# Kernel tuning notes

Measured on AMD Instinct MI355X. Metric: run time of the kernel, lower is better.

Reference implementation:

```python
import jax, jax.numpy as jnp
import numpy as np

NUM_NODES = 64
NUM_FEATURES = 256
OUTPUT_DIM = 256
BATCH_GRAPHS = 4096
TOTAL_ROWS = NUM_NODES * BATCH_GRAPHS


def setup_inputs() -> dict:
    key = jax.random.key(0)
    kx, kw = jax.random.split(key)
    x = jax.random.normal(kx, (TOTAL_ROWS, NUM_FEATURES), dtype=jnp.float32)
    # row i belongs to graph i // NUM_NODES (matches stride-num_nodes indexing in the module)
    batch = jnp.arange(TOTAL_ROWS, dtype=jnp.int64) // NUM_NODES
    # per-node linear weights: mlp[inode] is o3.Linear(256x0e -> 256x0e), bias-free
    W = jax.random.normal(kw, (NUM_NODES, NUM_FEATURES, OUTPUT_DIM), dtype=jnp.float32)
    return {"x": x, "batch": batch, "W": W}


def reference(x, batch, W):
    # x: [B*num_nodes, F]; W: [num_nodes, F, O]
    num_nodes, F, _ = W.shape
    B = x.shape[0] // num_nodes
    # node_features_reshape: out[b, :, inode] = x[inode + b*num_nodes] == reshape(B, num_nodes, F)
    xr = x.reshape(B, num_nodes, F)
    scale = 1.0 / jnp.sqrt(jnp.asarray(F, dtype=x.dtype))  # o3.Linear path normalization
    out = jnp.einsum("bnf,nfo->bno", xr, W) * scale  # per-node batched GEMM
    # scatter back: outs[inode + b*num_nodes] = out[b, inode] == reshape
    return out.reshape(B * num_nodes, -1)
```

## Files before the change

### kernel.cpp

```cpp
#include <hip/hip_runtime.h>
#include <stdint.h>

#define NODES   64
#define FDIM    256
#define ODIM    256
#define BGRAPH  4096
#define TROWS   (NODES * BGRAPH)

#define BM 64
#define BN 256
#define BK 32

typedef short  bf16x8  __attribute__((ext_vector_type(8)));
typedef float  floatx4 __attribute__((ext_vector_type(4)));

__device__ inline unsigned short f2bf(float f) {
    unsigned int u = __float_as_uint(f);
    return (unsigned short)((u + 0x7fffu + ((u >> 16) & 1u)) >> 16);
}

__global__ __launch_bounds__(256) void transpose_w(const float* __restrict__ W,
                                                   unsigned short* __restrict__ Wt) {
    __shared__ unsigned short t[64][65];
    const int node = blockIdx.y;
    const int tf = (blockIdx.x >> 2) << 6;
    const int to = (blockIdx.x & 3) << 6;
    const int tid = threadIdx.x;
    const float* Wn = W + node * (FDIM * ODIM);
#pragma unroll
    for (int i = 0; i < 16; ++i) {
        int flat = i * 256 + tid;
        int r = flat >> 6, c = flat & 63;
        float v = Wn[(tf + r) * ODIM + (to + c)] * 0.0625f;
        t[c][r] = f2bf(v);
    }
    __syncthreads();
    unsigned short* Wtn = Wt + node * (FDIM * ODIM);
#pragma unroll
    for (int i = 0; i < 16; ++i) {
        int flat = i * 256 + tid;
        int r = flat >> 6, c = flat & 63;
        Wtn[(to + r) * FDIM + (tf + c)] = t[r][c];
    }
}

__global__ __launch_bounds__(256) void gemm_node(const float* __restrict__ x,
                                                 const unsigned short* __restrict__ Wt,
                                                 float* __restrict__ out) {
    __shared__ unsigned short As[BM * BK];
    __shared__ unsigned short Bs[BN * BK];

    const int mblk = blockIdx.x;
    const int node = blockIdx.y;
    const int tid  = threadIdx.x;
    const int lane = tid & 63;
    const int wave = tid >> 6;
    const int wm   = wave >> 1;
    const int wn   = wave & 1;
    const int b0   = mblk * BM;

    const int l15 = lane & 15;
    const int l4  = lane >> 4;

    floatx4 acc[2][8] = {};

    const int arow0 = tid >> 3;
    const int ach0  = tid & 7;
    const int arow1 = (256 + tid) >> 3;
    const int ach1  = (256 + tid) & 7;
    const float* aptr0 = x + (((size_t)(b0 + arow0) * NODES + node) * FDIM + ach0 * 4);
    const float* aptr1 = x + (((size_t)(b0 + arow1) * NODES + node) * FDIM + ach1 * 4);

    const unsigned short* wt_node = Wt + (size_t)node * (ODIM * FDIM);

    for (int kt = 0; kt < 8; ++kt) {
        const int k0 = kt * BK;
        __syncthreads();

        {
            float4 v0 = *(const float4*)(aptr0 + k0);
            float4 v1 = *(const float4*)(aptr1 + k0);
            ushort4 p0, p1;
            p0.x = f2bf(v0.x); p0.y = f2bf(v0.y); p0.z = f2bf(v0.z); p0.w = f2bf(v0.w);
            p1.x = f2bf(v1.x); p1.y = f2bf(v1.y); p1.z = f2bf(v1.z); p1.w = f2bf(v1.w);
            *(ushort4*)(&As[arow0 * BK + ach0 * 4]) = p0;
            *(ushort4*)(&As[arow1 * BK + ach1 * 4]) = p1;
        }

#pragma unroll
        for (int j = 0; j < 4; ++j) {
            const int slot_base = (wave * 4 + j) * 64;
            const int slot = slot_base + lane;
            const unsigned short* g =
                wt_node + ((size_t)(slot >> 2) * FDIM + k0 + (slot & 3) * 8);
            __builtin_amdgcn_global_load_lds(
                (const __attribute__((address_space(1))) void*)g,
                (__attribute__((address_space(3))) void*)(&Bs[slot_base * 8]),
                16, 0, 0);
        }

        __syncthreads();

        bf16x8 a[2], b[8];
#pragma unroll
        for (int mi = 0; mi < 2; ++mi)
            a[mi] = *(const bf16x8*)(&As[(wm * 32 + mi * 16 + l15) * BK + l4 * 8]);
#pragma unroll
        for (int ni = 0; ni < 8; ++ni)
            b[ni] = *(const bf16x8*)(&Bs[(wn * 128 + ni * 16 + l15) * BK + l4 * 8]);
#pragma unroll
        for (int mi = 0; mi < 2; ++mi)
#pragma unroll
            for (int ni = 0; ni < 8; ++ni)
                acc[mi][ni] = __builtin_amdgcn_mfma_f32_16x16x32_bf16(a[mi], b[ni], acc[mi][ni], 0, 0, 0);
    }

#pragma unroll
    for (int mi = 0; mi < 2; ++mi) {
#pragma unroll
        for (int ni = 0; ni < 8; ++ni) {
            const int row_base = b0 + wm * 32 + mi * 16 + l4 * 4;
            const int col = wn * 128 + ni * 16 + l15;
#pragma unroll
            for (int r = 0; r < 4; ++r) {
                out[((size_t)(row_base + r) * NODES + node) * ODIM + col] = acc[mi][ni][r];
            }
        }
    }
}

__global__ __launch_bounds__(256) void naive_kernel(const float* __restrict__ x,
                                                    const float* __restrict__ W,
                                                    float* __restrict__ out) {
    __shared__ float xs[FDIM];
    const int row = blockIdx.x;
    const int node = row & (NODES - 1);
    const int o = threadIdx.x;
    xs[o] = x[(size_t)row * FDIM + o];
    __syncthreads();
    const float* Wn = W + (size_t)node * FDIM * ODIM;
    float s = 0.f;
#pragma unroll 8
    for (int f = 0; f < FDIM; ++f) s += xs[f] * Wn[(size_t)f * ODIM + o];
    out[(size_t)row * ODIM + o] = s * 0.0625f;
}

extern "C" void kernel_launch(void* const* d_in, const int* in_sizes, int n_in,
                              void* d_out, int out_size, void* d_ws, size_t ws_size,
                              hipStream_t stream) {
    const float* x = (const float*)d_in[0];
    const float* W = (const float*)d_in[2];
    float* out = (float*)d_out;

    const size_t wt_bytes = (size_t)NODES * ODIM * FDIM * sizeof(unsigned short);
    if (ws_size >= wt_bytes) {
        unsigned short* Wt = (unsigned short*)d_ws;
        transpose_w<<<dim3(16, NODES), 256, 0, stream>>>(W, Wt);
        gemm_node<<<dim3(BGRAPH / BM, NODES), 256, 0, stream>>>(x, Wt, out);
    } else {
        naive_kernel<<<dim3(TROWS), 256, 0, stream>>>(x, W, out);
    }
}
```

Baseline: 497.0 us.

## Double-buffer LDS tiles, enlarge M tile, swizzle B, and remap blocks per XCD

```diff
diff --git a/kernel.cpp b/kernel.cpp
--- a/kernel.cpp
+++ b/kernel.cpp
@@ -7,9 +7,10 @@
 #define BGRAPH  4096
 #define TROWS   (NODES * BGRAPH)
 
-#define BM 64
+#define BM 128
 #define BN 256
 #define BK 32
+#define ASTRIDE 40
 
 typedef short  bf16x8  __attribute__((ext_vector_type(8)));
 typedef float  floatx4 __attribute__((ext_vector_type(4)));
@@ -44,86 +45,126 @@
     }
 }
 
-__global__ __launch_bounds__(256) void gemm_node(const float* __restrict__ x,
-                                                 const unsigned short* __restrict__ Wt,
-                                                 float* __restrict__ out) {
-    __shared__ unsigned short As[BM * BK];
-    __shared__ unsigned short Bs[BN * BK];
-
-    const int mblk = blockIdx.x;
-    const int node = blockIdx.y;
+__global__ __launch_bounds__(256, 2) void gemm_node(const float* __restrict__ x,
+                                                    const unsigned short* __restrict__ Wt,
+                                                    float* __restrict__ out) {
+    __shared__ unsigned short As[2][BM * ASTRIDE];
+    __shared__ unsigned short Bs[2][BN * BK];
+
+    const int bid  = blockIdx.x;
+    const int xcd  = bid & 7;
+    const int jj   = bid >> 3;
+    const int node = xcd * 8 + (jj & 7);
+    const int mblk = jj >> 3;
+    const int b0   = mblk * BM;
+
     const int tid  = threadIdx.x;
     const int lane = tid & 63;
     const int wave = tid >> 6;
     const int wm   = wave >> 1;
     const int wn   = wave & 1;
-    const int b0   = mblk * BM;
-
-    const int l15 = lane & 15;
-    const int l4  = lane >> 4;
-
-    floatx4 acc[2][8] = {};
-
-    const int arow0 = tid >> 3;
-    const int ach0  = tid & 7;
-    const int arow1 = (256 + tid) >> 3;
-    const int ach1  = (256 + tid) & 7;
-    const float* aptr0 = x + (((size_t)(b0 + arow0) * NODES + node) * FDIM + ach0 * 4);
-    const float* aptr1 = x + (((size_t)(b0 + arow1) * NODES + node) * FDIM + ach1 * 4);
-
+    const int l15  = lane & 15;
+    const int l4   = lane >> 4;
+
+    const float* xblk = x + ((size_t)b0 * NODES + node) * FDIM;
     const unsigned short* wt_node = Wt + (size_t)node * (ODIM * FDIM);
 
+    int arow[4], ach[4];
+    size_t aoff[4];
+#pragma unroll
+    for (int i = 0; i < 4; ++i) {
+        int q = i * 256 + tid;
+        arow[i] = q >> 3;
+        ach[i]  = q & 7;
+        aoff[i] = (size_t)arow[i] * (NODES * FDIM) + ach[i] * 4;
+    }
+
+    floatx4 acc[4][8] = {};
+    float4 av[4];
+
+#pragma unroll
+    for (int i = 0; i < 4; ++i) av[i] = *(const float4*)(xblk + aoff[i]);
+#pragma unroll
+    for (int j = 0; j < 4; ++j) {
+        const int slot_base = (wave * 4 + j) * 64;
+        const int s = slot_base + lane;
+        const int o = s >> 2, c = s & 3;
+        const int jg = c ^ ((o >> 1) & 3);
+        const unsigned short* g = wt_node + (size_t)o * FDIM + jg * 8;
+        __builtin_amdgcn_global_load_lds(
+            (const __attribute__((address_space(1))) void*)g,
+            (__attribute__((address_space(3))) void*)(&Bs[0][slot_base * 8]),
+            16, 0, 0);
+    }
+#pragma unroll
+    for (int i = 0; i < 4; ++i) {
+        ushort4 p;
+        p.x = f2bf(av[i].x); p.y = f2bf(av[i].y); p.z = f2bf(av[i].z); p.w = f2bf(av[i].w);
+        *(ushort4*)(&As[0][arow[i] * ASTRIDE + ach[i] * 4]) = p;
+    }
+    __syncthreads();
+
+#pragma unroll
     for (int kt = 0; kt < 8; ++kt) {
-        const int k0 = kt * BK;
-        __syncthreads();
-
-        {
-            float4 v0 = *(const float4*)(aptr0 + k0);
-            float4 v1 = *(const float4*)(aptr1 + k0);
-            ushort4 p0, p1;
-            p0.x = f2bf(v0.x); p0.y = f2bf(v0.y); p0.z = f2bf(v0.z); p0.w = f2bf(v0.w);
-            p1.x = f2bf(v1.x); p1.y = f2bf(v1.y); p1.z = f2bf(v1.z); p1.w = f2bf(v1.w);
-            *(ushort4*)(&As[arow0 * BK + ach0 * 4]) = p0;
-            *(ushort4*)(&As[arow1 * BK + ach1 * 4]) = p1;
-        }
-
-#pragma unroll
-        for (int j = 0; j < 4; ++j) {
-            const int slot_base = (wave * 4 + j) * 64;
-            const int slot = slot_base + lane;
-            const unsigned short* g =
-                wt_node + ((size_t)(slot >> 2) * FDIM + k0 + (slot & 3) * 8);
-            __builtin_amdgcn_global_load_lds(
-                (const __attribute__((address_space(1))) void*)g,
-                (__attribute__((address_space(3))) void*)(&Bs[slot_base * 8]),
-                16, 0, 0);
-        }
-
-        __syncthreads();
-
-        bf16x8 a[2], b[8];
-#pragma unroll
-        for (int mi = 0; mi < 2; ++mi)
-            a[mi] = *(const bf16x8*)(&As[(wm * 32 + mi * 16 + l15) * BK + l4 * 8]);
-#pragma unroll
-        for (int ni = 0; ni < 8; ++ni)
-            b[ni] = *(const bf16x8*)(&Bs[(wn * 128 + ni * 16 + l15) * BK + l4 * 8]);
-#pragma unroll
-        for (int mi = 0; mi < 2; ++mi)
+        const int cur = kt & 1, nxt = cur ^ 1;
+        const int k1 = (kt + 1) * BK;
+
+        if (kt < 7) {
+#pragma unroll
+            for (int i = 0; i < 4; ++i) av[i] = *(const float4*)(xblk + aoff[i] + k1);
+#pragma unroll
+            for (int j = 0; j < 4; ++j) {
+                const int slot_base = (wave * 4 + j) * 64;
+                const int s = slot_base + lane;
+                const int o = s >> 2, c = s & 3;
+                const int jg = c ^ ((o >> 1) & 3);
+                const unsigned short* g = wt_node + (size_t)o * FDIM + k1 + jg * 8;
+                __builtin_amdgcn_global_load_lds(
+                    (const __attribute__((address_space(1))) void*)g,
+                    (__attribute__((address_space(3))) void*)(&Bs[nxt][slot_base * 8]),
+                    16, 0, 0);
+            }
+        }
+
+        bf16x8 a[4], b[8];
+#pragma unroll
+        for (int mi = 0; mi < 4; ++mi) {
+            const int m = wm * 64 + mi * 16 + l15;
+            a[mi] = *(const bf16x8*)(&As[cur][m * ASTRIDE + l4 * 8]);
+        }
+#pragma unroll
+        for (int ni = 0; ni < 8; ++ni) {
+            const int n = wn * 128 + ni * 16 + l15;
+            b[ni] = *(const bf16x8*)(&Bs[cur][n * 32 + (l4 ^ ((n >> 1) & 3)) * 8]);
+        }
+
+#pragma unroll
+        for (int mi = 0; mi < 4; ++mi)
 #pragma unroll
             for (int ni = 0; ni < 8; ++ni)
                 acc[mi][ni] = __builtin_amdgcn_mfma_f32_16x16x32_bf16(a[mi], b[ni], acc[mi][ni], 0, 0, 0);
-    }
-
-#pragma unroll
-    for (int mi = 0; mi < 2; ++mi) {
+
+        if (kt < 7) {
+#pragma unroll
+            for (int i = 0; i < 4; ++i) {
+                ushort4 p;
+                p.x = f2bf(av[i].x); p.y = f2bf(av[i].y); p.z = f2bf(av[i].z); p.w = f2bf(av[i].w);
+                *(ushort4*)(&As[nxt][arow[i] * ASTRIDE + ach[i] * 4]) = p;
+            }
+            __syncthreads();
+        }
+    }
+
+    float* outblk = out + ((size_t)b0 * NODES + node) * ODIM;
+#pragma unroll
+    for (int mi = 0; mi < 4; ++mi) {
+        const int row_base = wm * 64 + mi * 16 + l4 * 4;
 #pragma unroll
         for (int ni = 0; ni < 8; ++ni) {
-            const int row_base = b0 + wm * 32 + mi * 16 + l4 * 4;
             const int col = wn * 128 + ni * 16 + l15;
 #pragma unroll
             for (int r = 0; r < 4; ++r) {
-                out[((size_t)(row_base + r) * NODES + node) * ODIM + col] = acc[mi][ni][r];
+                outblk[(size_t)(row_base + r) * (NODES * ODIM) + col] = acc[mi][ni][r];
             }
         }
     }
@@ -156,7 +197,7 @@
     if (ws_size >= wt_bytes) {
         unsigned short* Wt = (unsigned short*)d_ws;
         transpose_w<<<dim3(16, NODES), 256, 0, stream>>>(W, Wt);
-        gemm_node<<<dim3(BGRAPH / BM, NODES), 256, 0, stream>>>(x, Wt, out);
+        gemm_node<<<dim3((BGRAPH / BM) * NODES), 256, 0, stream>>>(x, Wt, out);
     } else {
         naive_kernel<<<dim3(TROWS), 256, 0, stream>>>(x, W, out);
     }
```

After: 464.2 us. 1.07x faster.
